# Kernel optimization log

Measured on AMD Instinct MI355X. Metric: run time of the kernel, lower is better.

The kernel has to match this reference:

```python
import jax, jax.numpy as jnp
import numpy as np

B, S, E, NH = 2, 2048, 512, 4
DH = E // NH  # 128
KSZ = 4      # causal conv kernel size


def setup_inputs() -> dict:
    key = jax.random.key(0)
    ks = jax.random.split(key, 12)
    hw_std = (2.0 / 5.0 / DH) ** 0.5
    return {
        "x": jax.random.normal(ks[0], (B, S, E), jnp.float32),
        "W_up": jax.random.normal(ks[1], (2 * E, E), jnp.float32) * 0.02,
        "Wq": jax.random.normal(ks[2], (NH, DH, DH), jnp.float32) * hw_std,
        "Wk": jax.random.normal(ks[3], (NH, DH, DH), jnp.float32) * hw_std,
        "Wv": jax.random.normal(ks[4], (NH, DH, DH), jnp.float32) * hw_std,
        "conv_w": jax.random.normal(ks[5], (E, E, KSZ), jnp.float32) * (1.0 / (E * KSZ) ** 0.5),
        "conv_b": jnp.zeros((E,), jnp.float32),
        "Wi": jax.random.normal(ks[6], (NH, 3 * E), jnp.float32) * 0.01,
        "bi": jax.random.normal(ks[7], (NH,), jnp.float32) * 0.1,
        "Wf": jax.random.normal(ks[8], (NH, 3 * E), jnp.float32) * 0.01,
        "bf": jax.random.normal(ks[9], (NH,), jnp.float32),
        "skip": jnp.ones((E,), jnp.float32),
        "W_down": jax.random.normal(ks[10], (E, E), jnp.float32) * 0.02,
        "b_down": jnp.zeros((E,), jnp.float32),
    }


def _headwise(u, W):
    # LinearHeadwiseExpand: x -> [B,S,NH,dh] @ [NH,od,dh]
    b, s, e = u.shape
    nh = W.shape[0]
    uh = u.reshape(b, s, nh, -1)
    return jnp.einsum('bshd,hod->bsho', uh, W).reshape(b, s, e)


def reference(x, W_up, Wq, Wk, Wv, conv_w, conv_b, Wi, bi, Wf, bf, skip, W_down, b_down):
    b, s, e = x.shape
    nh = Wq.shape[0]
    dh = e // nh
    eps = 1e-6

    x_inner = x @ W_up.T                        # [B,S,2E]
    x_mlstm, z = jnp.split(x_inner, 2, axis=-1)

    # causal conv1d: left-pad kernel_size-1, trim implicit via padding spec
    xc = jnp.transpose(x_mlstm, (0, 2, 1))      # [B,E,S]
    conv = jax.lax.conv_general_dilated(
        xc, conv_w, window_strides=(1,), padding=[(KSZ - 1, 0)],
        dimension_numbers=('NCH', 'OIH', 'NCH')) + conv_b[None, :, None]
    x_conv_act = jax.nn.silu(jnp.transpose(conv, (0, 2, 1)))  # [B,S,E]

    q = _headwise(x_conv_act, Wq)
    k = _headwise(x_conv_act, Wk)
    v = _headwise(x_mlstm, Wv)

    gate_in = jnp.concatenate([q, k, v], axis=-1)           # [B,S,3E]
    igate = jnp.transpose(gate_in @ Wi.T + bi, (0, 2, 1))   # [B,NH,S]
    fgate = jnp.transpose(gate_in @ Wf.T + bf, (0, 2, 1))   # [B,NH,S]

    qh = jnp.transpose(q.reshape(b, s, nh, dh), (0, 2, 1, 3))  # [B,NH,S,DH]
    kh = jnp.transpose(k.reshape(b, s, nh, dh), (0, 2, 1, 3))
    vh = jnp.transpose(v.reshape(b, s, nh, dh), (0, 2, 1, 3))

    # log-space cumulative forget-gate D matrix
    log_fg = jax.nn.log_sigmoid(fgate)                      # [B,NH,S]
    lfc = jnp.cumsum(log_fg, axis=-1)                       # [B,NH,S]
    log_fg_mat = lfc[..., :, None] - lfc[..., None, :]      # [B,NH,S,S]
    mask = jnp.tril(jnp.ones((s, s), bool))
    log_fg_mat = jnp.where(mask, log_fg_mat, -jnp.inf)
    log_D = log_fg_mat + igate[..., None, :]                # + igate[j]

    max_log_D = jnp.max(log_D, axis=-1, keepdims=True)      # rowwise stabilize
    Dm = jnp.exp(log_D - max_log_D)

    qk = jnp.einsum('bhsd,bhtd->bhst', qh, kh) / (dh ** 0.5)
    C = qk * Dm
    normalizer = jnp.maximum(jnp.abs(jnp.sum(C, axis=-1, keepdims=True)),
                             jnp.exp(-max_log_D))
    Cn = C / (normalizer + eps)
    h = jnp.einsum('bhst,bhtd->bhsd', Cn, vh)               # [B,NH,S,DH]

    # MultiHeadLayerNorm = group_norm(num_groups=NH, no affine, eps=1e-5)
    ht = jnp.transpose(h, (0, 2, 1, 3))                     # [B,S,NH,DH]
    mean = jnp.mean(ht, axis=-1, keepdims=True)
    var = jnp.var(ht, axis=-1, keepdims=True)
    h_norm = ((ht - mean) / jnp.sqrt(var + 1e-5)).reshape(b, s, e)

    h_skip = h_norm + skip * x_conv_act
    h_state = h_skip * jax.nn.silu(z)
    return h_state @ W_down.T + b_down
```

## Files before the change

kernel.cpp:

```cpp
#include <hip/hip_runtime.h>
#include <hip/hip_bf16.h>
#include <math.h>

typedef __hip_bfloat16 bf16;
typedef unsigned short ushort_t;
typedef __bf16 v8bf __attribute__((ext_vector_type(8)));
typedef float v4f __attribute__((ext_vector_type(4)));

#define B_   2
#define S_   2048
#define E_   512
#define NH_  4
#define DH_  128
#define NIN_ 14
#define NSPLIT_ 4

__device__ inline ushort_t f2bf(float f) {
  union { float f; unsigned u; } v; v.f = f;
  unsigned r = (v.u + 0x7FFFu + ((v.u >> 16) & 1u)) >> 16;
  return (ushort_t)r;
}
__device__ inline float bf2f(ushort_t u) {
  union { unsigned uu; float ff; } c; c.uu = (unsigned)u << 16; return c.ff;
}

struct CvtArgs {
  const void* src[NIN_];
  float* dst[NIN_];
  ushort_t* bdst[NIN_];
  int sz[NIN_];
};

__global__ __launch_bounds__(256) void convert_all(CvtArgs a, const unsigned* modew) {
  const bool isbf = (*modew == 0x3F803F80u);
  const int t = blockIdx.y;
  const int n = a.sz[t];
  const int base = blockIdx.x * 1024 + threadIdx.x;
  const float* sf = (const float*)a.src[t];
  const bf16*  sb = (const bf16*)a.src[t];
  const ushort_t* su = (const ushort_t*)a.src[t];
  float* d = a.dst[t];
  ushort_t* bd = a.bdst[t];
#pragma unroll
  for (int k = 0; k < 4; ++k) {
    int idx = base + k * 256;
    if (idx < n) {
      float f = isbf ? __bfloat162float(sb[idx]) : sf[idx];
      if (d)  d[idx] = f;
      if (bd) bd[idx] = isbf ? su[idx] : f2bf(f);
    }
  }
}

__global__ __launch_bounds__(256) void conv_repack(
    const void* __restrict__ src, ushort_t* __restrict__ Wt, const unsigned* __restrict__ modew)
{
  const bool isbf = (*modew == 0x3F803F80u);
  int idx = blockIdx.x * 256 + threadIdx.x;
  if (idx < E_ * E_ * 4) {
    int k = idx & 3, i = (idx >> 2) & (E_ - 1), o = idx >> 11;
    ushort_t v;
    if (isbf) v = ((const ushort_t*)src)[idx];
    else      v = f2bf(((const float*)src)[idx]);
    Wt[((size_t)k * E_ + o) * E_ + i] = v;
  }
}

__global__ __launch_bounds__(256) void gates_repack(
    const void* __restrict__ wi, const void* __restrict__ wf,
    ushort_t* __restrict__ Wgh, ushort_t* __restrict__ Wgl,
    const unsigned* __restrict__ modew)
{
  const bool isbf = (*modew == 0x3F803F80u);
  int idx = blockIdx.x * 256 + threadIdx.x;
  if (idx < 16 * 3 * E_) {
    int row = idx / (3 * E_), col = idx % (3 * E_);
    float w = 0.f;
    if (row < 4)      w = isbf ? bf2f(((const ushort_t*)wi)[row * 3 * E_ + col])
                               : ((const float*)wi)[row * 3 * E_ + col];
    else if (row < 8) w = isbf ? bf2f(((const ushort_t*)wf)[(row - 4) * 3 * E_ + col])
                               : ((const float*)wf)[(row - 4) * 3 * E_ + col];
    ushort_t hi = f2bf(w);
    Wgh[idx] = hi;
    Wgl[idx] = f2bf(w - bf2f(hi));
  }
}

template <int NT, bool HAS_BIAS, bool OUT_BF16, bool OUT_LO, bool OUT_DUAL>
__global__ __launch_bounds__(128, 4) void gemm2(
    const ushort_t* __restrict__ A, int lda,
    const ushort_t* __restrict__ Bm, int ldb,
    const float* __restrict__ bias,
    ushort_t* __restrict__ Cb, ushort_t* __restrict__ Cl,
    void* __restrict__ Cd, int ldc,
    int M, int K, const unsigned* __restrict__ modew)
{
  const int nm = M >> 6;
  const int m0 = (blockIdx.x % nm) << 6;
  const int n0 = (blockIdx.x / nm) * (NT * 16);
  const int tid = threadIdx.x;
  const int wv = tid >> 6, lane = tid & 63;
  const int ln15 = lane & 15, quad = lane >> 4;
  const int mA = m0 + wv * 16 + ln15;
  const int mB = mA + 32;
  v4f accA[NT], accB[NT];
#pragma unroll
  for (int i = 0; i < NT; ++i) { accA[i] = (v4f){0,0,0,0}; accB[i] = (v4f){0,0,0,0}; }
  const ushort_t* arowA = A + (size_t)mA * lda + quad * 8;
  const ushort_t* arowB = A + (size_t)mB * lda + quad * 8;
  const ushort_t* brow = Bm + (size_t)(n0 + ln15) * ldb + quad * 8;
  for (int k0 = 0; k0 < K; k0 += 32) {
    v8bf aA = *(const v8bf*)(arowA + k0);
    v8bf aB = *(const v8bf*)(arowB + k0);
#pragma unroll
    for (int nt = 0; nt < NT; ++nt) {
      v8bf b = *(const v8bf*)(brow + (size_t)nt * 16 * ldb + k0);
      accA[nt] = __builtin_amdgcn_mfma_f32_16x16x32_bf16(aA, b, accA[nt], 0, 0, 0);
      accB[nt] = __builtin_amdgcn_mfma_f32_16x16x32_bf16(aB, b, accB[nt], 0, 0, 0);
    }
  }
  bool obf = false;
  if (OUT_DUAL) obf = (*modew == 0x3F803F80u);
#pragma unroll
  for (int half = 0; half < 2; ++half) {
    const v4f* acc = half ? accB : accA;
#pragma unroll
    for (int nt = 0; nt < NT; ++nt) {
#pragma unroll
      for (int rr = 0; rr < 4; ++rr) {
        int m = m0 + wv * 16 + half * 32 + quad * 4 + rr;
        int n = n0 + nt * 16 + ln15;
        float c = acc[nt][rr];
        if (HAS_BIAS) c += bias[n];
        size_t off = (size_t)m * ldc + n;
        if (OUT_BF16) {
          ushort_t hi = f2bf(c);
          Cb[off] = hi;
          if (OUT_LO) Cl[off] = f2bf(c - bf2f(hi));
        }
        if (OUT_DUAL) {
          if (obf) ((bf16*)Cd)[off] = __float2bfloat16(c);
          else     ((float*)Cd)[off] = c;
        }
      }
    }
  }
}

__global__ __launch_bounds__(256, 2) void conv_lds2(
    const ushort_t* __restrict__ xhi,
    const ushort_t* __restrict__ xlo,
    const ushort_t* __restrict__ Wt,
    const float* __restrict__ cb,
    float* __restrict__ xca,
    ushort_t* __restrict__ xcab)
{
  const int m0 = (blockIdx.x & 63) << 6;
  const int n0 = (blockIdx.x >> 6) << 6;
  const int tid = threadIdx.x;
  const int wv = tid >> 6;
  const int lane = tid & 63;
  const int ln15 = lane & 15, quad = lane >> 4;
  const bool boundary = (m0 & (S_ - 1)) == 0;

  constexpr int LP = 132;
  __shared__ ushort_t Ab[2][68 * LP];

  int srow[17], scol[17], sstr[17];
#pragma unroll
  for (int j = 0; j < 17; ++j) {
    int idx = j * 256 + tid;
    sstr[j] = idx / 2176;
    int rem = idx - sstr[j] * 2176;
    srow[j] = rem >> 5;
    scol[j] = (rem & 31) << 2;
  }
  ushort4 sreg[17];
  auto stage_load = [&](int c) {
#pragma unroll
    for (int j = 0; j < 17; ++j) {
      const ushort_t* src = sstr[j] ? xlo : xhi;
      sreg[j] = *(const ushort4*)(src + (ptrdiff_t)(m0 - 4 + srow[j]) * (2 * E_)
                                  + c * 128 + scol[j]);
    }
    if (boundary) {
#pragma unroll
      for (int j = 0; j < 17; ++j)
        if (srow[j] < 4) sreg[j] = make_ushort4(0, 0, 0, 0);
    }
  };
  auto stage_write = [&]() {
#pragma unroll
    for (int j = 0; j < 17; ++j)
      *(ushort4*)&Ab[sstr[j]][srow[j] * LP + scol[j]] = sreg[j];
  };

  v4f acc[4];
#pragma unroll
  for (int i = 0; i < 4; ++i) acc[i] = (v4f){0, 0, 0, 0};

  v8bf breg[16];
  auto loadB = [&](int c) {
    const ushort_t* bw = Wt + (size_t)(n0 + wv * 16 + ln15) * E_ + c * 128 + quad * 8;
#pragma unroll
    for (int t = 0; t < 4; ++t)
#pragma unroll
      for (int k0 = 0; k0 < 4; ++k0)
        breg[t * 4 + k0] = *(const v8bf*)(bw + (size_t)t * E_ * E_ + k0 * 32);
  };
  auto compute = [&]() {
#pragma unroll
    for (int t = 0; t < 4; ++t) {
#pragma unroll
      for (int k0 = 0; k0 < 4; ++k0) {
#pragma unroll
        for (int rt = 0; rt < 4; ++rt) {
          const int ro = (rt * 16 + ln15 + t + 1) * LP + k0 * 32 + quad * 8;
          v8bf a1 = *(const v8bf*)&Ab[0][ro];
          v8bf a2 = *(const v8bf*)&Ab[1][ro];
          acc[rt] = __builtin_amdgcn_mfma_f32_16x16x32_bf16(a1, breg[t * 4 + k0], acc[rt], 0, 0, 0);
          acc[rt] = __builtin_amdgcn_mfma_f32_16x16x32_bf16(a2, breg[t * 4 + k0], acc[rt], 0, 0, 0);
        }
      }
    }
  };

  stage_load(0);
  stage_write();
  __syncthreads();
#pragma unroll
  for (int c = 0; c < 4; ++c) {
    if (c < 3) stage_load(c + 1);
    loadB(c);
    compute();
    if (c < 3) {
      __syncthreads();
      stage_write();
      __syncthreads();
    }
  }

  const int col = n0 + wv * 16 + ln15;
  const float cbv = cb[col];
#pragma unroll
  for (int rt = 0; rt < 4; ++rt) {
#pragma unroll
    for (int rr = 0; rr < 4; ++rr) {
      const int row = m0 + rt * 16 + quad * 4 + rr;
      float c = acc[rt][rr] + cbv;
      float r = c / (1.f + __expf(-c));
      const size_t off = (size_t)row * E_ + col;
      xca[off] = r;
      xcab[off] = f2bf(r);
    }
  }
}

__global__ __launch_bounds__(256) void qkv_mfma(
    const ushort_t* __restrict__ xcab,
    const ushort_t* __restrict__ xmb,
    const ushort_t* __restrict__ wqb, const ushort_t* __restrict__ wkb, const ushort_t* __restrict__ wvb,
    ushort_t* __restrict__ qb, ushort_t* __restrict__ kb, ushort_t* __restrict__ vb,
    ushort_t* __restrict__ vtb)
{
  const int type = blockIdx.y >> 2;
  const int h = blockIdx.y & 3;
  const int m0 = blockIdx.x << 6;
  const int tid = threadIdx.x;
  const int wv = tid >> 6, lane = tid & 63;
  const int ln15 = lane & 15, quad = lane >> 4;

  const ushort_t* Asrc = (type == 2) ? (xmb + h * DH_) : (xcab + h * DH_);
  const int lda = (type == 2) ? (2 * E_) : E_;
  const ushort_t* W = ((type == 0) ? wqb : (type == 1) ? wkb : wvb) + (size_t)h * DH_ * DH_;
  ushort_t* dst = (type == 0) ? qb : (type == 1) ? kb : vb;

  v4f acc[8];
#pragma unroll
  for (int i = 0; i < 8; ++i) acc[i] = (v4f){0.f, 0.f, 0.f, 0.f};

  const ushort_t* arow = Asrc + (size_t)(m0 + wv * 16 + ln15) * lda + quad * 8;
  const ushort_t* brow = W + (size_t)ln15 * DH_ + quad * 8;
#pragma unroll
  for (int c = 0; c < 4; ++c) {
    v8bf a = *(const v8bf*)(arow + c * 32);
#pragma unroll
    for (int nt = 0; nt < 8; ++nt) {
      v8bf b = *(const v8bf*)(brow + (size_t)nt * 16 * DH_ + c * 32);
      acc[nt] = __builtin_amdgcn_mfma_f32_16x16x32_bf16(a, b, acc[nt], 0, 0, 0);
    }
  }
  const int bb = m0 >> 11;
  const int s0 = (m0 & (S_ - 1)) + wv * 16 + quad * 4;
#pragma unroll
  for (int nt = 0; nt < 8; ++nt) {
    ushort_t pk[4];
#pragma unroll
    for (int rr = 0; rr < 4; ++rr) {
      int m = m0 + wv * 16 + quad * 4 + rr;
      int s = m & (S_ - 1);
      int n = nt * 16 + ln15;
      ushort_t u = f2bf(acc[nt][rr]);
      pk[rr] = u;
      dst[((size_t)(bb * NH_ + h) * S_ + s) * DH_ + n] = u;
    }
    if (type == 2) {
      *(ushort4*)&vtb[((size_t)(bb * NH_ + h) * DH_ + nt * 16 + ln15) * S_ + s0] =
          make_ushort4(pk[0], pk[1], pk[2], pk[3]);
    }
  }
}

__global__ __launch_bounds__(64) void gates_mfma(
    const ushort_t* __restrict__ qb, const ushort_t* __restrict__ kb, const ushort_t* __restrict__ vb,
    const ushort_t* __restrict__ Wgh, const ushort_t* __restrict__ Wgl,
    const float* __restrict__ bi, const float* __restrict__ bfp,
    float* __restrict__ ig, float* __restrict__ fgo)
{
  const int m0 = blockIdx.x << 4;
  const int lane = threadIdx.x;
  const int ln15 = lane & 15, quad = lane >> 4;
  const int m = m0 + ln15;
  const int b = m >> 11, s = m & (S_ - 1);
  const size_t base0 = ((size_t)(b * NH_) * S_ + s) * DH_;

  v4f acc = (v4f){0.f, 0.f, 0.f, 0.f};
  const ushort_t* wh = Wgh + (size_t)ln15 * (3 * E_) + quad * 8;
  const ushort_t* wl = Wgl + (size_t)ln15 * (3 * E_) + quad * 8;
#pragma unroll
  for (int kk = 0; kk < 48; ++kk) {
    const int kg = kk * 32 + quad * 8;
    const int type = kg >> 9;
    const int h = (kg >> 7) & 3;
    const int d = kg & 127;
    const ushort_t* src = (type == 0) ? qb : (type == 1) ? kb : vb;
    v8bf a = *(const v8bf*)(src + base0 + (size_t)h * S_ * DH_ + d);
    v8bf bh2 = *(const v8bf*)(wh + kk * 32);
    v8bf bl2 = *(const v8bf*)(wl + kk * 32);
    acc = __builtin_amdgcn_mfma_f32_16x16x32_bf16(a, bh2, acc, 0, 0, 0);
    acc = __builtin_amdgcn_mfma_f32_16x16x32_bf16(a, bl2, acc, 0, 0, 0);
  }
  if (ln15 < 8) {
#pragma unroll
    for (int r = 0; r < 4; ++r) {
      int mm = m0 + quad * 4 + r;
      int bb2 = mm >> 11, ss = mm & (S_ - 1);
      if (ln15 < 4) ig [((size_t)(bb2 * NH_ + ln15)) * S_ + ss]       = acc[r] + bi[ln15];
      else          fgo[((size_t)(bb2 * NH_ + (ln15 - 4))) * S_ + ss] = acc[r] + bfp[ln15 - 4];
    }
  }
}

__global__ __launch_bounds__(256) void gate_scan(
    const float* __restrict__ fgv, const float* __restrict__ igv,
    float* __restrict__ lfc, float* __restrict__ gout, float* __restrict__ Mout)
{
  const int bh = blockIdx.x;
  const int tid = threadIdx.x;
  const float* f = fgv + (size_t)bh * S_;
  const float* ii = igv + (size_t)bh * S_;
  __shared__ float sb[256];
  float loc[8];
  float run = 0.f;
#pragma unroll
  for (int j = 0; j < 8; ++j) {
    float x = f[tid * 8 + j];
    float ls = (x >= 0.f) ? -log1pf(expf(-x)) : (x - log1pf(expf(x)));
    run += ls; loc[j] = run;
  }
  sb[tid] = run; __syncthreads();
  for (int off = 1; off < 256; off <<= 1) {
    float t = (tid >= off) ? sb[tid - off] : 0.f;
    __syncthreads();
    sb[tid] += t;
    __syncthreads();
  }
  float pre = (tid > 0) ? sb[tid - 1] : 0.f;
  float lv[8], gl[8];
  float mrun = -INFINITY;
#pragma unroll
  for (int j = 0; j < 8; ++j) {
    lv[j] = pre + loc[j];
    lfc[(size_t)bh * S_ + tid * 8 + j] = lv[j];
    float gg = ii[tid * 8 + j] - lv[j];
    gout[(size_t)bh * S_ + tid * 8 + j] = gg;
    mrun = fmaxf(mrun, gg); gl[j] = mrun;
  }
  __syncthreads();
  sb[tid] = mrun; __syncthreads();
  for (int off = 1; off < 256; off <<= 1) {
    float t = (tid >= off) ? sb[tid - off] : -INFINITY;
    __syncthreads();
    sb[tid] = fmaxf(sb[tid], t);
    __syncthreads();
  }
  float mpre = (tid > 0) ? sb[tid - 1] : -INFINITY;
#pragma unroll
  for (int j = 0; j < 8; ++j)
    Mout[(size_t)bh * S_ + tid * 8 + j] = fmaxf(mpre, gl[j]);
}

__global__ __launch_bounds__(256, 2) void attn_split(
    const ushort_t* __restrict__ qb, const ushort_t* __restrict__ kb,
    const ushort_t* __restrict__ vtb,
    const float* __restrict__ gv, const float* __restrict__ Mv,
    float* __restrict__ pbuf,
    float* __restrict__ pcs)
{
  const int bh = blockIdx.x & 7;
  const int j = (blockIdx.x >> 3) & 15;
  const int chunk = blockIdx.x >> 7;
  const ushort_t* q = qb + (size_t)bh * S_ * DH_;
  const ushort_t* k = kb + (size_t)bh * S_ * DH_;
  const ushort_t* vt = vtb + (size_t)bh * DH_ * S_;
  const float* gp = gv + (size_t)bh * S_;
  const float* Mp = Mv + (size_t)bh * S_;

  __shared__ ushort_t Ps[4][2][16][72];

  const int tid = threadIdx.x;
  const int wv = tid >> 6;
  const int lane = tid & 63;
  const int ln15 = lane & 15;
  const int quad = lane >> 4;
  const int rowLo = (j * 4 + wv) * 16;
  const int rowHi = rowLo + 1024;
  const float lrs = 2.4245772f;

  ushort_t (*PsLo)[72] = Ps[wv][0];
  ushort_t (*PsHi)[72] = Ps[wv][1];

  v8bf qfL[4], qfH[4];
#pragma unroll
  for (int c = 0; c < 4; ++c) {
    qfL[c] = *(const v8bf*)(q + (size_t)(rowLo + ln15) * DH_ + c * 32 + quad * 8);
    qfH[c] = *(const v8bf*)(q + (size_t)(rowHi + ln15) * DH_ + c * 32 + quad * 8);
  }
  float MrL[4], MrH[4];
#pragma unroll
  for (int r = 0; r < 4; ++r) {
    MrL[r] = Mp[rowLo + quad * 4 + r] + lrs;
    MrH[r] = Mp[rowHi + quad * 4 + r] + lrs;
  }

  v4f haccL[8], haccH[8];
#pragma unroll
  for (int i = 0; i < 8; ++i) { haccL[i] = (v4f){0,0,0,0}; haccH[i] = (v4f){0,0,0,0}; }
  float csL[4] = {0,0,0,0}, csH[4] = {0,0,0,0};

  const int NI = 17 + j;
  const int it0 = (chunk * NI) / NSPLIT_;
  const int it1 = ((chunk + 1) * NI) / NSPLIT_;

  for (int it = it0; it < it1; ++it) {
    const int t0 = it << 6;
    const bool full2  = (t0 + 63 <= rowLo);
    const bool anyLo  = (t0 <= rowLo + 15);
    const bool fullHi = (t0 + 63 <= rowHi);

    if (full2) {
      v8bf kf[4][4];
#pragma unroll
      for (int tt = 0; tt < 4; ++tt) {
        const ushort_t* kr = k + (size_t)(t0 + tt * 16 + ln15) * DH_ + quad * 8;
#pragma unroll
        for (int c = 0; c < 4; ++c) kf[tt][c] = *(const v8bf*)(kr + c * 32);
      }
      v8bf vf0[8];
#pragma unroll
      for (int dt = 0; dt < 8; ++dt)
        vf0[dt] = *(const v8bf*)(vt + (size_t)(dt * 16 + ln15) * S_ + t0 + quad * 8);
#pragma unroll
      for (int tt = 0; tt < 4; ++tt) {
        v4f sL = (v4f){0,0,0,0}, sH = (v4f){0,0,0,0};
#pragma unroll
        for (int c = 0; c < 4; ++c) {
          sH = __builtin_amdgcn_mfma_f32_16x16x32_bf16(qfH[c], kf[tt][c], sH, 0, 0, 0);
          sL = __builtin_amdgcn_mfma_f32_16x16x32_bf16(qfL[c], kf[tt][c], sL, 0, 0, 0);
        }
        const float gt = gp[t0 + tt * 16 + ln15];
#pragma unroll
        for (int r = 0; r < 4; ++r) {
          float pH = sH[r] * __expf(fminf(gt - MrH[r], 60.f));
          float pL = sL[r] * __expf(fminf(gt - MrL[r], 60.f));
          csH[r] += pH; csL[r] += pL;
          PsHi[quad * 4 + r][tt * 16 + ln15] = f2bf(pH);
          PsLo[quad * 4 + r][tt * 16 + ln15] = f2bf(pL);
        }
      }
      {
        v8bf vf1[8];
#pragma unroll
        for (int dt = 0; dt < 8; ++dt)
          vf1[dt] = *(const v8bf*)(vt + (size_t)(dt * 16 + ln15) * S_ + t0 + 32 + quad * 8);
        v8bf pfH0 = *(const v8bf*)&PsHi[ln15][quad * 8];
        v8bf pfL0 = *(const v8bf*)&PsLo[ln15][quad * 8];
#pragma unroll
        for (int dt = 0; dt < 8; ++dt) {
          haccH[dt] = __builtin_amdgcn_mfma_f32_16x16x32_bf16(pfH0, vf0[dt], haccH[dt], 0, 0, 0);
          haccL[dt] = __builtin_amdgcn_mfma_f32_16x16x32_bf16(pfL0, vf0[dt], haccL[dt], 0, 0, 0);
        }
        v8bf pfH1 = *(const v8bf*)&PsHi[ln15][32 + quad * 8];
        v8bf pfL1 = *(const v8bf*)&PsLo[ln15][32 + quad * 8];
#pragma unroll
        for (int dt = 0; dt < 8; ++dt) {
          haccH[dt] = __builtin_amdgcn_mfma_f32_16x16x32_bf16(pfH1, vf1[dt], haccH[dt], 0, 0, 0);
          haccL[dt] = __builtin_amdgcn_mfma_f32_16x16x32_bf16(pfL1, vf1[dt], haccL[dt], 0, 0, 0);
        }
      }
    } else if (!anyLo && fullHi) {
      v8bf kf[4][4];
#pragma unroll
      for (int tt = 0; tt < 4; ++tt) {
        const ushort_t* kr = k + (size_t)(t0 + tt * 16 + ln15) * DH_ + quad * 8;
#pragma unroll
        for (int c = 0; c < 4; ++c) kf[tt][c] = *(const v8bf*)(kr + c * 32);
      }
      v8bf vf0[8];
#pragma unroll
      for (int dt = 0; dt < 8; ++dt)
        vf0[dt] = *(const v8bf*)(vt + (size_t)(dt * 16 + ln15) * S_ + t0 + quad * 8);
#pragma unroll
      for (int tt = 0; tt < 4; ++tt) {
        v4f sH = (v4f){0,0,0,0};
#pragma unroll
        for (int c = 0; c < 4; ++c)
          sH = __builtin_amdgcn_mfma_f32_16x16x32_bf16(qfH[c], kf[tt][c], sH, 0, 0, 0);
        const float gt = gp[t0 + tt * 16 + ln15];
#pragma unroll
        for (int r = 0; r < 4; ++r) {
          float pH = sH[r] * __expf(fminf(gt - MrH[r], 60.f));
          csH[r] += pH;
          PsHi[quad * 4 + r][tt * 16 + ln15] = f2bf(pH);
        }
      }
      {
        v8bf vf1[8];
#pragma unroll
        for (int dt = 0; dt < 8; ++dt)
          vf1[dt] = *(const v8bf*)(vt + (size_t)(dt * 16 + ln15) * S_ + t0 + 32 + quad * 8);
        v8bf pfH0 = *(const v8bf*)&PsHi[ln15][quad * 8];
#pragma unroll
        for (int dt = 0; dt < 8; ++dt)
          haccH[dt] = __builtin_amdgcn_mfma_f32_16x16x32_bf16(pfH0, vf0[dt], haccH[dt], 0, 0, 0);
        v8bf pfH1 = *(const v8bf*)&PsHi[ln15][32 + quad * 8];
#pragma unroll
        for (int dt = 0; dt < 8; ++dt)
          haccH[dt] = __builtin_amdgcn_mfma_f32_16x16x32_bf16(pfH1, vf1[dt], haccH[dt], 0, 0, 0);
      }
    } else {
      const bool loIter = anyLo;
#pragma unroll
      for (int tt = 0; tt < 4; ++tt) {
        const int tg0 = t0 + tt * 16;
        const bool hv = (tg0 <= rowHi + 15);
        const bool lv = (tg0 <= rowLo + 15);
        if (hv) {
          v4f sL = (v4f){0,0,0,0}, sH = (v4f){0,0,0,0};
          const ushort_t* kr = k + (size_t)(tg0 + ln15) * DH_ + quad * 8;
          if (lv) {
#pragma unroll
            for (int c = 0; c < 4; ++c) {
              v8bf kf = *(const v8bf*)(kr + c * 32);
              sH = __builtin_amdgcn_mfma_f32_16x16x32_bf16(qfH[c], kf, sH, 0, 0, 0);
              sL = __builtin_amdgcn_mfma_f32_16x16x32_bf16(qfL[c], kf, sL, 0, 0, 0);
            }
          } else {
#pragma unroll
            for (int c = 0; c < 4; ++c) {
              v8bf kf = *(const v8bf*)(kr + c * 32);
              sH = __builtin_amdgcn_mfma_f32_16x16x32_bf16(qfH[c], kf, sH, 0, 0, 0);
            }
          }
          const int tg = tg0 + ln15;
          const float gt = gp[tg];
#pragma unroll
          for (int r = 0; r < 4; ++r) {
            const int rowH = rowHi + quad * 4 + r;
            float p = sH[r] * __expf(fminf(gt - MrH[r], 60.f));
            p = (tg <= rowH) ? p : 0.f;
            csH[r] += p;
            PsHi[quad * 4 + r][tt * 16 + ln15] = f2bf(p);
          }
          if (lv) {
#pragma unroll
            for (int r = 0; r < 4; ++r) {
              const int rowL = rowLo + quad * 4 + r;
              float p = sL[r] * __expf(fminf(gt - MrL[r], 60.f));
              p = (tg <= rowL) ? p : 0.f;
              csL[r] += p;
              PsLo[quad * 4 + r][tt * 16 + ln15] = f2bf(p);
            }
          } else if (loIter) {
#pragma unroll
            for (int r = 0; r < 4; ++r) PsLo[quad * 4 + r][tt * 16 + ln15] = 0;
          }
        } else {
#pragma unroll
          for (int r = 0; r < 4; ++r) PsHi[quad * 4 + r][tt * 16 + ln15] = 0;
          if (loIter) {
#pragma unroll
            for (int r = 0; r < 4; ++r) PsLo[quad * 4 + r][tt * 16 + ln15] = 0;
          }
        }
      }
#pragma unroll
      for (int c2 = 0; c2 < 2; ++c2) {
        v8bf pfH = *(const v8bf*)&PsHi[ln15][c2 * 32 + quad * 8];
        if (loIter) {
          v8bf pfL = *(const v8bf*)&PsLo[ln15][c2 * 32 + quad * 8];
#pragma unroll
          for (int dt = 0; dt < 8; ++dt) {
            v8bf vf = *(const v8bf*)(vt + (size_t)(dt * 16 + ln15) * S_ + t0 + c2 * 32 + quad * 8);
            haccH[dt] = __builtin_amdgcn_mfma_f32_16x16x32_bf16(pfH, vf, haccH[dt], 0, 0, 0);
            haccL[dt] = __builtin_amdgcn_mfma_f32_16x16x32_bf16(pfL, vf, haccL[dt], 0, 0, 0);
          }
        } else {
#pragma unroll
          for (int dt = 0; dt < 8; ++dt) {
            v8bf vf = *(const v8bf*)(vt + (size_t)(dt * 16 + ln15) * S_ + t0 + c2 * 32 + quad * 8);
            haccH[dt] = __builtin_amdgcn_mfma_f32_16x16x32_bf16(pfH, vf, haccH[dt], 0, 0, 0);
          }
        }
      }
    }
  }

#pragma unroll
  for (int r = 0; r < 4; ++r) {
    float a = csL[r], b2 = csH[r];
    a += __shfl_xor(a, 1, 64);  b2 += __shfl_xor(b2, 1, 64);
    a += __shfl_xor(a, 2, 64);  b2 += __shfl_xor(b2, 2, 64);
    a += __shfl_xor(a, 4, 64);  b2 += __shfl_xor(b2, 4, 64);
    a += __shfl_xor(a, 8, 64);  b2 += __shfl_xor(b2, 8, 64);
    csL[r] = a; csH[r] = b2;
  }
  const size_t slab = (size_t)(chunk * 8 + bh);
  if (ln15 == 0) {
#pragma unroll
    for (int r = 0; r < 4; ++r) {
      __builtin_nontemporal_store(csL[r], &pcs[slab * S_ + rowLo + quad * 4 + r]);
      __builtin_nontemporal_store(csH[r], &pcs[slab * S_ + rowHi + quad * 4 + r]);
    }
  }
#pragma unroll
  for (int dt = 0; dt < 8; ++dt) {
#pragma unroll
    for (int r = 0; r < 4; ++r) {
      __builtin_nontemporal_store(haccL[dt][r],
          &pbuf[(slab * S_ + rowLo + quad * 4 + r) * DH_ + dt * 16 + ln15]);
      __builtin_nontemporal_store(haccH[dt][r],
          &pbuf[(slab * S_ + rowHi + quad * 4 + r) * DH_ + dt * 16 + ln15]);
    }
  }
}

__global__ __launch_bounds__(256) void gn_fused(
    const float* __restrict__ pbuf, const float* __restrict__ pcs,
    const float* __restrict__ Mv, const float* __restrict__ lfcv,
    const float* __restrict__ xca,
    const ushort_t* __restrict__ xhib, const ushort_t* __restrict__ xlob,
    const float* __restrict__ skip,
    ushort_t* __restrict__ hsb)
{
  const int row = blockIdx.x;
  const int b = row >> 11, s2 = row & (S_ - 1);
  const int tid = threadIdx.x;
  const int hd = tid >> 6, lane = tid & 63;
  const int bh = b * NH_ + hd;

  float v0 = 0.f, v1 = 0.f, cs = 0.f;
#pragma unroll
  for (int c = 0; c < NSPLIT_; ++c) {
    const size_t base = ((size_t)(c * 8 + bh) * S_ + s2) * DH_;
    v0 += __builtin_nontemporal_load(&pbuf[base + lane]);
    v1 += __builtin_nontemporal_load(&pbuf[base + lane + 64]);
    cs += __builtin_nontemporal_load(&pcs[(size_t)(c * 8 + bh) * S_ + s2]);
  }
  const size_t off = (size_t)bh * S_ + s2;
  const float floorv = __expf(fminf(-(lfcv[off] + Mv[off]), 80.f));
  const float inv = 1.f / (fmaxf(fabsf(cs), floorv) + 1e-6f);
  v0 *= inv; v1 *= inv;

  float s = v0 + v1, q = v0 * v0 + v1 * v1;
  for (int o = 32; o > 0; o >>= 1) { s += __shfl_down(s, o, 64); q += __shfl_down(q, o, 64); }
  s = __shfl(s, 0, 64); q = __shfl(q, 0, 64);
  float mean = s * (1.f / 128.f);
  float var = q * (1.f / 128.f) - mean * mean;
  float rstd = rsqrtf(fmaxf(var, 0.f) + 1e-5f);
#pragma unroll
  for (int t2 = 0; t2 < 2; ++t2) {
    int e = hd * DH_ + lane + t2 * 64;
    float hv = (t2 == 0) ? v0 : v1;
    float hn = (hv - mean) * rstd;
    float hs = hn + skip[e] * xca[(size_t)row * E_ + e];
    size_t zoff = (size_t)row * (2 * E_) + E_ + e;
    float z = bf2f(xhib[zoff]) + bf2f(xlob[zoff]);
    float sz = z / (1.f + __expf(-z));
    hsb[(size_t)row * E_ + e] = f2bf(hs * sz);
  }
}

extern "C" void kernel_launch(void* const* d_in, const int* in_sizes, int n_in,
                              void* d_out, int out_size, void* d_ws, size_t ws_size,
                              hipStream_t stream) {
  (void)out_size; (void)ws_size; (void)n_in;
  const unsigned* modew = (const unsigned*)d_in[11];

  float* ws = (float*)d_ws;
  size_t cur = 0;
  auto allocf = [&](size_t n) { float* p = ws + cur; cur += (n + 3) & ~(size_t)3; return p; };
  auto allocb = [&](size_t n) { return (ushort_t*)allocf((n + 1) / 2); };

  const bool needf[NIN_] = {false,false,false,false,false,false,true,false,true,false,true,true,false,true};
  const bool needb[NIN_] = {true,true,true,true,true,false,false,false,false,false,false,false,true,false};

  float* cvf[NIN_];
  ushort_t* cvb[NIN_];
  CvtArgs ca;
  int maxsz = 0;
  for (int i = 0; i < NIN_; ++i) {
    cvf[i] = needf[i] ? allocf((size_t)in_sizes[i]) : nullptr;
    cvb[i] = needb[i] ? allocb((size_t)in_sizes[i]) : nullptr;
    ca.src[i] = d_in[i];
    ca.dst[i] = cvf[i];
    ca.bdst[i] = cvb[i];
    ca.sz[i] = in_sizes[i];
    if (in_sizes[i] > maxsz) maxsz = in_sizes[i];
  }

  const size_t nBS = (size_t)B_ * S_;
  ushort_t* Wtc      = allocb((size_t)4 * E_ * E_);
  ushort_t* Wgh      = allocb((size_t)16 * 3 * E_);
  ushort_t* Wgl      = allocb((size_t)16 * 3 * E_);
  ushort_t* x_innerb = allocb(nBS * 2 * E_);
  ushort_t* x_lob    = allocb(nBS * 2 * E_);
  float* xca         = allocf(nBS * E_);
  ushort_t* xcab     = allocb(nBS * E_);
  ushort_t* qbuf     = allocb(nBS * E_);
  ushort_t* kbuf     = allocb(nBS * E_);
  ushort_t* vbuf     = allocb(nBS * E_);
  ushort_t* vtbuf    = allocb(nBS * E_);
  float* ig      = allocf((size_t)B_ * NH_ * S_);
  float* fg      = allocf((size_t)B_ * NH_ * S_);
  float* lfc     = allocf((size_t)B_ * NH_ * S_);
  float* gbuf    = allocf((size_t)B_ * NH_ * S_);
  float* Mbuf    = allocf((size_t)B_ * NH_ * S_);
  float* pbuf    = allocf((size_t)NSPLIT_ * 8 * S_ * DH_);
  float* pcs     = allocf((size_t)NSPLIT_ * 8 * S_);
  ushort_t* hsb  = allocb(nBS * E_);

  convert_all<<<dim3((maxsz + 1023) / 1024, NIN_), 256, 0, stream>>>(ca, modew);
  conv_repack<<<dim3((E_ * E_ * 4 + 255) / 256), 256, 0, stream>>>(d_in[5], Wtc, modew);
  gates_repack<<<dim3((16 * 3 * E_ + 255) / 256), 256, 0, stream>>>(d_in[7], d_in[9], Wgh, Wgl, modew);
  gemm2<4, false, true, true, false><<<dim3(64 * (1024 / 64)), 128, 0, stream>>>(
      cvb[0], E_, cvb[1], E_, nullptr, x_innerb, x_lob, nullptr, 2 * E_, 4096, E_, modew);
  conv_lds2<<<dim3(64 * 8), 256, 0, stream>>>(x_innerb, x_lob, Wtc, cvf[6], xca, xcab);
  qkv_mfma<<<dim3(4096 / 64, 12), 256, 0, stream>>>(xcab, x_innerb, cvb[2], cvb[3], cvb[4],
                                                    qbuf, kbuf, vbuf, vtbuf);
  gates_mfma<<<dim3(4096 / 16), 64, 0, stream>>>(qbuf, kbuf, vbuf, Wgh, Wgl,
                                                 cvf[8], cvf[10], ig, fg);
  gate_scan<<<dim3(B_ * NH_), 256, 0, stream>>>(fg, ig, lfc, gbuf, Mbuf);
  attn_split<<<dim3(16 * NSPLIT_ * 8), 256, 0, stream>>>(
      qbuf, kbuf, vtbuf, gbuf, Mbuf, pbuf, pcs);
  gn_fused<<<dim3(4096), 256, 0, stream>>>(pbuf, pcs, Mbuf, lfc, xca, x_innerb, x_lob,
                                           cvf[11], hsb);
  gemm2<4, true, false, false, true><<<dim3(64 * (512 / 64)), 128, 0, stream>>>(
      hsb, E_, cvb[12], E_, cvf[13], nullptr, nullptr, d_out, E_, 4096, E_, modew);
}
```

Before: 292.8 us.

## Stage GEMM A tiles through LDS with register-prefetched double staging

Replaces the direct-from-global register GEMM with a 256-thread kernel that stages 64x128 A chunks into padded shared memory, prefetching the next chunk into registers while computing the current one. Each wave keeps its B fragment in registers and reads the A rows from LDS, so A is fetched from global once per block instead of once per wave. This is applied to both the up-projection and the down-projection GEMMs. In exchange it adds two barriers per K chunk and more register pressure.

```diff
diff --git a/kernel.cpp b/kernel.cpp
--- a/kernel.cpp
+++ b/kernel.cpp
@@ -86,62 +86,101 @@
   }
 }
 
-template <int NT, bool HAS_BIAS, bool OUT_BF16, bool OUT_LO, bool OUT_DUAL>
-__global__ __launch_bounds__(128, 4) void gemm2(
-    const ushort_t* __restrict__ A, int lda,
-    const ushort_t* __restrict__ Bm, int ldb,
+template <bool HAS_BIAS, bool OUT_BF16, bool OUT_LO, bool OUT_DUAL>
+__global__ __launch_bounds__(256, 4) void gemm_lds(
+    const ushort_t* __restrict__ A,
+    const ushort_t* __restrict__ Bm,
     const float* __restrict__ bias,
     ushort_t* __restrict__ Cb, ushort_t* __restrict__ Cl,
     void* __restrict__ Cd, int ldc,
-    int M, int K, const unsigned* __restrict__ modew)
+    const unsigned* __restrict__ modew)
 {
-  const int nm = M >> 6;
-  const int m0 = (blockIdx.x % nm) << 6;
-  const int n0 = (blockIdx.x / nm) * (NT * 16);
+  const int m0 = (blockIdx.x & 63) << 6;
+  const int n0 = (blockIdx.x >> 6) << 6;
   const int tid = threadIdx.x;
-  const int wv = tid >> 6, lane = tid & 63;
+  const int wv = tid >> 6;
+  const int lane = tid & 63;
   const int ln15 = lane & 15, quad = lane >> 4;
-  const int mA = m0 + wv * 16 + ln15;
-  const int mB = mA + 32;
-  v4f accA[NT], accB[NT];
-#pragma unroll
-  for (int i = 0; i < NT; ++i) { accA[i] = (v4f){0,0,0,0}; accB[i] = (v4f){0,0,0,0}; }
-  const ushort_t* arowA = A + (size_t)mA * lda + quad * 8;
-  const ushort_t* arowB = A + (size_t)mB * lda + quad * 8;
-  const ushort_t* brow = Bm + (size_t)(n0 + ln15) * ldb + quad * 8;
-  for (int k0 = 0; k0 < K; k0 += 32) {
-    v8bf aA = *(const v8bf*)(arowA + k0);
-    v8bf aB = *(const v8bf*)(arowB + k0);
-#pragma unroll
-    for (int nt = 0; nt < NT; ++nt) {
-      v8bf b = *(const v8bf*)(brow + (size_t)nt * 16 * ldb + k0);
-      accA[nt] = __builtin_amdgcn_mfma_f32_16x16x32_bf16(aA, b, accA[nt], 0, 0, 0);
-      accB[nt] = __builtin_amdgcn_mfma_f32_16x16x32_bf16(aB, b, accB[nt], 0, 0, 0);
-    }
-  }
+
+  constexpr int LP = 132;
+  __shared__ ushort_t Ab[64 * LP];
+
+  int srow[8], scol[8];
+#pragma unroll
+  for (int j = 0; j < 8; ++j) {
+    int idx = j * 256 + tid;
+    srow[j] = idx >> 5;
+    scol[j] = (idx & 31) << 2;
+  }
+  ushort4 sreg[8];
+  auto stage_load = [&](int c) {
+#pragma unroll
+    for (int j = 0; j < 8; ++j)
+      sreg[j] = *(const ushort4*)(A + (size_t)(m0 + srow[j]) * E_ + c * 128 + scol[j]);
+  };
+  auto stage_write = [&]() {
+#pragma unroll
+    for (int j = 0; j < 8; ++j)
+      *(ushort4*)&Ab[srow[j] * LP + scol[j]] = sreg[j];
+  };
+
+  v4f acc[4];
+#pragma unroll
+  for (int i = 0; i < 4; ++i) acc[i] = (v4f){0, 0, 0, 0};
+
+  v8bf breg[4];
+  auto loadB = [&](int c) {
+    const ushort_t* bw = Bm + (size_t)(n0 + wv * 16 + ln15) * E_ + c * 128 + quad * 8;
+#pragma unroll
+    for (int k0 = 0; k0 < 4; ++k0)
+      breg[k0] = *(const v8bf*)(bw + k0 * 32);
+  };
+  auto compute = [&]() {
+#pragma unroll
+    for (int k0 = 0; k0 < 4; ++k0) {
+#pragma unroll
+      for (int rt = 0; rt < 4; ++rt) {
+        v8bf a = *(const v8bf*)&Ab[(rt * 16 + ln15) * LP + k0 * 32 + quad * 8];
+        acc[rt] = __builtin_amdgcn_mfma_f32_16x16x32_bf16(a, breg[k0], acc[rt], 0, 0, 0);
+      }
+    }
+  };
+
+  stage_load(0);
+  stage_write();
+  __syncthreads();
+#pragma unroll
+  for (int c = 0; c < 4; ++c) {
+    if (c < 3) stage_load(c + 1);
+    loadB(c);
+    compute();
+    if (c < 3) {
+      __syncthreads();
+      stage_write();
+      __syncthreads();
+    }
+  }
+
   bool obf = false;
   if (OUT_DUAL) obf = (*modew == 0x3F803F80u);
-#pragma unroll
-  for (int half = 0; half < 2; ++half) {
-    const v4f* acc = half ? accB : accA;
-#pragma unroll
-    for (int nt = 0; nt < NT; ++nt) {
-#pragma unroll
-      for (int rr = 0; rr < 4; ++rr) {
-        int m = m0 + wv * 16 + half * 32 + quad * 4 + rr;
-        int n = n0 + nt * 16 + ln15;
-        float c = acc[nt][rr];
-        if (HAS_BIAS) c += bias[n];
-        size_t off = (size_t)m * ldc + n;
-        if (OUT_BF16) {
-          ushort_t hi = f2bf(c);
-          Cb[off] = hi;
-          if (OUT_LO) Cl[off] = f2bf(c - bf2f(hi));
-        }
-        if (OUT_DUAL) {
-          if (obf) ((bf16*)Cd)[off] = __float2bfloat16(c);
-          else     ((float*)Cd)[off] = c;
-        }
+  const int col = n0 + wv * 16 + ln15;
+  float bv = 0.f;
+  if (HAS_BIAS) bv = bias[col];
+#pragma unroll
+  for (int rt = 0; rt < 4; ++rt) {
+#pragma unroll
+    for (int rr = 0; rr < 4; ++rr) {
+      const int row = m0 + rt * 16 + quad * 4 + rr;
+      float c = acc[rt][rr] + bv;
+      const size_t off = (size_t)row * ldc + col;
+      if (OUT_BF16) {
+        ushort_t hi = f2bf(c);
+        Cb[off] = hi;
+        if (OUT_LO) Cl[off] = f2bf(c - bf2f(hi));
+      }
+      if (OUT_DUAL) {
+        if (obf) ((bf16*)Cd)[off] = __float2bfloat16(c);
+        else     ((float*)Cd)[off] = c;
       }
     }
   }
@@ -753,8 +792,8 @@
   convert_all<<<dim3((maxsz + 1023) / 1024, NIN_), 256, 0, stream>>>(ca, modew);
   conv_repack<<<dim3((E_ * E_ * 4 + 255) / 256), 256, 0, stream>>>(d_in[5], Wtc, modew);
   gates_repack<<<dim3((16 * 3 * E_ + 255) / 256), 256, 0, stream>>>(d_in[7], d_in[9], Wgh, Wgl, modew);
-  gemm2<4, false, true, true, false><<<dim3(64 * (1024 / 64)), 128, 0, stream>>>(
-      cvb[0], E_, cvb[1], E_, nullptr, x_innerb, x_lob, nullptr, 2 * E_, 4096, E_, modew);
+  gemm_lds<false, true, true, false><<<dim3(64 * 16), 256, 0, stream>>>(
+      cvb[0], cvb[1], nullptr, x_innerb, x_lob, nullptr, 2 * E_, modew);
   conv_lds2<<<dim3(64 * 8), 256, 0, stream>>>(x_innerb, x_lob, Wtc, cvf[6], xca, xcab);
   qkv_mfma<<<dim3(4096 / 64, 12), 256, 0, stream>>>(xcab, x_innerb, cvb[2], cvb[3], cvb[4],
                                                     qbuf, kbuf, vbuf, vtbuf);
@@ -765,6 +804,6 @@
       qbuf, kbuf, vtbuf, gbuf, Mbuf, pbuf, pcs);
   gn_fused<<<dim3(4096), 256, 0, stream>>>(pbuf, pcs, Mbuf, lfc, xca, x_innerb, x_lob,
                                            cvf[11], hsb);
-  gemm2<4, true, false, false, true><<<dim3(64 * (512 / 64)), 128, 0, stream>>>(
-      hsb, E_, cvb[12], E_, cvf[13], nullptr, nullptr, d_out, E_, 4096, E_, modew);
-}
+  gemm_lds<true, false, false, true><<<dim3(64 * 8), 256, 0, stream>>>(
+      hsb, cvb[12], cvf[13], nullptr, nullptr, d_out, E_, modew);
+}
```

Result: faster. 264.5 us (-9.7%).
